# Kernel tuning notes

Hardware: AMD Instinct MI355X
Metric: run time of the kernel (lower is better)

The kernel has to match this reference:

```python
import jax, jax.numpy as jnp
import numpy as np

B, NQ, NK, DQ, DK, DV, H = 8, 256, 512, 256, 256, 256, 64
NEG = -1e6


def setup_inputs() -> dict:
    key = jax.random.key(0)
    k1, k2, k3, k4, k5, k6, k7 = jax.random.split(key, 7)
    return {
        "queries": jax.random.normal(k1, (B, NQ, DQ), dtype=jnp.float32),
        "keys": jax.random.normal(k2, (B, NK, DK), dtype=jnp.float32),
        "values": jax.random.normal(k3, (B, NK, DV), dtype=jnp.float32),
        "valid_lens": jax.random.randint(k4, (B,), 1, NK + 1),
        "Wq": jax.random.normal(k5, (DQ, H), dtype=jnp.float32) / np.sqrt(DQ),
        "Wk": jax.random.normal(k6, (DK, H), dtype=jnp.float32) / np.sqrt(DK),
        "wv": jax.random.normal(k7, (H,), dtype=jnp.float32) / np.sqrt(H),
    }


def reference(queries, keys, values, valid_lens, Wq, Wk, wv):
    # project: [B,NQ,H], [B,NK,H]
    q = jnp.einsum("bqd,dh->bqh", queries, Wq)
    k = jnp.einsum("bkd,dh->bkh", keys, Wk)
    # additive features: [B,NQ,NK,H] -> tanh -> reduce with w_v -> scores [B,NQ,NK]
    features = jnp.tanh(q[:, :, None, :] + k[:, None, :, :])
    scores = jnp.einsum("bqkh,h->bqk", features, wv)
    # masked softmax over key axis (per-batch valid_lens)
    mask = jnp.arange(NK)[None, None, :] < valid_lens[:, None, None]
    scores = jnp.where(mask, scores, NEG)
    attn = jax.nn.softmax(scores, axis=-1)
    # dropout p=0 (eval) -> identity; weighted sum of values [B,NQ,DV]
    return jnp.einsum("bqk,bkv->bqv", attn, values)
```

## Files before the change

kernel.cpp:

```cpp
#include <hip/hip_runtime.h>
#include <hip/hip_bf16.h>

constexpr int B  = 8;
constexpr int NQ = 256;
constexpr int NK = 512;
constexpr int D  = 256;
constexpr int DV = 256;
constexpr int H  = 64;
constexpr float LOG2E = 1.4426950408889634f;
constexpr float CSCALE = 2.f * LOG2E;

constexpr int RPB = 32;

__global__ __launch_bounds__(512) void proj_kernel(
    const float* __restrict__ queries, const float* __restrict__ keys,
    const float* __restrict__ Wq, const float* __restrict__ Wk,
    float* __restrict__ qp, float* __restrict__ kp)
{
    const int r0 = blockIdx.x * RPB;
    const bool isQ = (r0 < B * NQ);
    const float* src = isQ ? queries + (size_t)r0 * D
                           : keys + (size_t)(r0 - B * NQ) * D;
    const float* W   = isQ ? Wq : Wk;
    float* out       = isQ ? qp + (size_t)r0 * H
                           : kp + (size_t)(r0 - B * NQ) * H;

    __shared__ __align__(16) float rows[RPB][D];
#pragma unroll
    for (int j = 0; j < 4; ++j)
        ((float4*)&rows[0][0])[threadIdx.x + j * 512] =
            ((const float4*)src)[threadIdx.x + j * 512];
    __syncthreads();

    const int h = threadIdx.x & 63;
    const int g = threadIdx.x >> 6;
    float s0 = 0.f, s1 = 0.f, s2 = 0.f, s3 = 0.f;
#pragma unroll 2
    for (int d4 = 0; d4 < D / 4; ++d4) {
        float w0 = W[(d4 * 4 + 0) * H + h];
        float w1 = W[(d4 * 4 + 1) * H + h];
        float w2 = W[(d4 * 4 + 2) * H + h];
        float w3 = W[(d4 * 4 + 3) * H + h];
        float4 ra = *(const float4*)&rows[g][d4 * 4];
        float4 rb = *(const float4*)&rows[g + 8][d4 * 4];
        float4 rc = *(const float4*)&rows[g + 16][d4 * 4];
        float4 rd = *(const float4*)&rows[g + 24][d4 * 4];
        s0 = fmaf(ra.x, w0, s0);  s1 = fmaf(rb.x, w0, s1);
        s2 = fmaf(rc.x, w0, s2);  s3 = fmaf(rd.x, w0, s3);
        s0 = fmaf(ra.y, w1, s0);  s1 = fmaf(rb.y, w1, s1);
        s2 = fmaf(rc.y, w1, s2);  s3 = fmaf(rd.y, w1, s3);
        s0 = fmaf(ra.z, w2, s0);  s1 = fmaf(rb.z, w2, s1);
        s2 = fmaf(rc.z, w2, s2);  s3 = fmaf(rd.z, w2, s3);
        s0 = fmaf(ra.w, w3, s0);  s1 = fmaf(rb.w, w3, s1);
        s2 = fmaf(rc.w, w3, s2);  s3 = fmaf(rd.w, w3, s3);
    }
    out[g * H + h]         = s0 * CSCALE;
    out[(g + 8) * H + h]   = s1 * CSCALE;
    out[(g + 16) * H + h]  = s2 * CSCALE;
    out[(g + 24) * H + h]  = s3 * CSCALE;
}

constexpr int KT   = 128;
constexpr int KPAD = 68;
constexpr int QPB  = 8;

#define FMA2(acc, a, v) \
    acc.x = fmaf(a, v.x, acc.x); acc.y = fmaf(a, v.y, acc.y);
#define AVQ(acc, aq) \
    FMA2(acc, aq.x, v0) FMA2(acc, aq.y, v1) FMA2(acc, aq.z, v2) FMA2(acc, aq.w, v3)

__global__ __launch_bounds__(1024, 4) void attn_kernel(
    const float* __restrict__ qp, const float* __restrict__ kp,
    const float* __restrict__ values, const int* __restrict__ valid_lens,
    const float* __restrict__ wv, float* __restrict__ out)
{
    const int b    = blockIdx.x & 7;
    const int q0   = (blockIdx.x >> 3) * QPB;
    const int t    = threadIdx.x;
    const int w    = t >> 6;
    const int l    = t & 63;
    const int qloc = w >> 1;
    const int half = w & 1;

    __shared__ __align__(16) float kT[KT * KPAD];
    __shared__ __align__(16) float qv[QPB][H];
    __shared__ __align__(16) float w2[H];
    __shared__ __align__(16) float rq[QPB];
    __shared__ __align__(16) float sc[QPB][NK];

    if (half == 0)
        qv[qloc][l] = qp[((size_t)b * NQ + q0 + qloc) * H + l];

    const float wvl = wv[l];
    float swv = wvl;
#pragma unroll
    for (int off = 32; off > 0; off >>= 1) swv += __shfl_xor(swv, off);
    if (w == 0) w2[l] = -2.f * wvl;

    const int vlen = valid_lens[b];
    const int ntl  = (vlen + KT - 1) / KT;

    for (int kt = ntl; kt < NK / KT; ++kt)
        sc[qloc][kt * KT + half * 64 + l] = 0.f;

    const float* kb = kp + (size_t)b * NK * H;
    float4 r0 = ((const float4*)kb)[t];
    float4 r1 = ((const float4*)kb)[t + 1024];

    for (int kt = 0; kt < ntl; ++kt) {
        __syncthreads();
        {
            int i4 = t;
            *(float4*)&kT[(i4 >> 4) * KPAD + (i4 & 15) * 4] = r0;
            i4 = t + 1024;
            *(float4*)&kT[(i4 >> 4) * KPAD + (i4 & 15) * 4] = r1;
        }
        if (kt + 1 < ntl) {
            const float* nsrc = kb + (size_t)(kt + 1) * KT * H;
            r0 = ((const float4*)nsrc)[t];
            r1 = ((const float4*)nsrc)[t + 1024];
        }
        __syncthreads();

        const int kg = kt * KT + half * 64 + l;
        if (kt * KT + half * 64 < vlen) {
            const float* qrow = &qv[qloc][0];
            const float* krow = &kT[(half * 64 + l) * KPAD];
            float s0 = 0.f;
#pragma unroll
            for (int h4 = 0; h4 < H / 4; ++h4) {
                float4 qq = *(const float4*)&qrow[h4 * 4];
                float4 ww = *(const float4*)&w2[h4 * 4];
                float4 kk = *(const float4*)&krow[h4 * 4];
                float Ax = __builtin_amdgcn_exp2f(qq.x + kk.x) + 1.f;
                float Ay = __builtin_amdgcn_exp2f(qq.y + kk.y) + 1.f;
                float Az = __builtin_amdgcn_exp2f(qq.z + kk.z) + 1.f;
                float Aw = __builtin_amdgcn_exp2f(qq.w + kk.w) + 1.f;
                float n1 = fmaf(ww.x, Ay, ww.y * Ax);
                float d1 = Ax * Ay;
                float n2 = fmaf(ww.z, Aw, ww.w * Az);
                float d2 = Az * Aw;
                float nq = fmaf(n1, d2, n2 * d1);
                float dq = d1 * d2;
                s0 = fmaf(nq, __builtin_amdgcn_rcpf(dq), s0);
            }
            sc[qloc][kg] = (kg < vlen)
                ? __builtin_amdgcn_exp2f((s0 + swv) * LOG2E) : 0.f;
        } else {
            sc[qloc][kg] = 0.f;
        }
    }
    __syncthreads();

    float sum = 0.f;
#pragma unroll
    for (int j = 0; j < 8; ++j) sum += sc[qloc][l + j * 64];
#pragma unroll
    for (int off = 32; off > 0; off >>= 1) sum += __shfl_xor(sum, off);
    if (half == 0 && l == 0) rq[qloc] = __builtin_amdgcn_rcpf(sum);

    float2 acc0{0,0}, acc1{0,0}, acc2{0,0}, acc3{0,0};
    float2 acc4{0,0}, acc5{0,0}, acc6{0,0}, acc7{0,0};
    const float* Vb = values + (size_t)b * NK * DV + half * 128 + 2 * l;
    const int nchunks = (vlen + 3) >> 2;
    for (int c = qloc; c < nchunks; c += 8) {
        const int k = 4 * c;
        float4 a0 = *(const float4*)&sc[0][k];
        float4 a1 = *(const float4*)&sc[1][k];
        float4 a2 = *(const float4*)&sc[2][k];
        float4 a3 = *(const float4*)&sc[3][k];
        float4 a4 = *(const float4*)&sc[4][k];
        float4 a5 = *(const float4*)&sc[5][k];
        float4 a6 = *(const float4*)&sc[6][k];
        float4 a7 = *(const float4*)&sc[7][k];
        const float* vr = Vb + (size_t)k * DV;
        float2 v0 = *(const float2*)(vr);
        float2 v1 = *(const float2*)(vr + DV);
        float2 v2 = *(const float2*)(vr + 2 * DV);
        float2 v3 = *(const float2*)(vr + 3 * DV);
        AVQ(acc0, a0) AVQ(acc1, a1) AVQ(acc2, a2) AVQ(acc3, a3)
        AVQ(acc4, a4) AVQ(acc5, a5) AVQ(acc6, a6) AVQ(acc7, a7)
    }

    float* pt = kT;
    const int pbase = qloc * 4 * 256 + half * 128 + 2 * l;
    *(float2*)&pt[pbase + 0 * 256] = acc0;
    *(float2*)&pt[pbase + 1 * 256] = acc1;
    *(float2*)&pt[pbase + 2 * 256] = acc2;
    *(float2*)&pt[pbase + 3 * 256] = acc3;
    __syncthreads();
    if (w < 4) {
        float4 r{0,0,0,0};
#pragma unroll
        for (int p = 0; p < 8; ++p) {
            float4 x = *(const float4*)&pt[(p * 4 + w) * 256 + 4 * l];
            r.x += x.x; r.y += x.y; r.z += x.z; r.w += x.w;
        }
        const float s = rq[w];
        r.x *= s; r.y *= s; r.z *= s; r.w *= s;
        *(float4*)&out[((size_t)b * NQ + q0 + w) * DV + 4 * l] = r;
    }
    __syncthreads();
    *(float2*)&pt[pbase + 0 * 256] = acc4;
    *(float2*)&pt[pbase + 1 * 256] = acc5;
    *(float2*)&pt[pbase + 2 * 256] = acc6;
    *(float2*)&pt[pbase + 3 * 256] = acc7;
    __syncthreads();
    if (w < 4) {
        float4 r{0,0,0,0};
#pragma unroll
        for (int p = 0; p < 8; ++p) {
            float4 x = *(const float4*)&pt[(p * 4 + w) * 256 + 4 * l];
            r.x += x.x; r.y += x.y; r.z += x.z; r.w += x.w;
        }
        const float s = rq[4 + w];
        r.x *= s; r.y *= s; r.z *= s; r.w *= s;
        *(float4*)&out[((size_t)b * NQ + q0 + 4 + w) * DV + 4 * l] = r;
    }
}

extern "C" void kernel_launch(void* const* d_in, const int* in_sizes, int n_in,
                              void* d_out, int out_size, void* d_ws, size_t ws_size,
                              hipStream_t stream) {
    const float* queries    = (const float*)d_in[0];
    const float* keys       = (const float*)d_in[1];
    const float* values     = (const float*)d_in[2];
    const int*   valid_lens = (const int*)d_in[3];
    const float* Wq         = (const float*)d_in[4];
    const float* Wk         = (const float*)d_in[5];
    const float* wv         = (const float*)d_in[6];
    float* out = (float*)d_out;

    float* qp = (float*)d_ws;
    float* kp = qp + (size_t)B * NQ * H;

    proj_kernel<<<(B * NQ + B * NK) / RPB, 512, 0, stream>>>(
        queries, keys, Wq, Wk, qp, kp);

    attn_kernel<<<B * (NQ / QPB), 1024, 0, stream>>>(
        qp, kp, values, valid_lens, wv, out);
}
```

Before: 103.2 us.

## Interleave attention-value accumulation with score tiles and simplify tanh reduction

```diff
diff --git a/kernel.cpp b/kernel.cpp
--- a/kernel.cpp
+++ b/kernel.cpp
@@ -35,7 +35,7 @@
     const int h = threadIdx.x & 63;
     const int g = threadIdx.x >> 6;
     float s0 = 0.f, s1 = 0.f, s2 = 0.f, s3 = 0.f;
-#pragma unroll 2
+#pragma unroll 4
     for (int d4 = 0; d4 < D / 4; ++d4) {
         float w0 = W[(d4 * 4 + 0) * H + h];
         float w1 = W[(d4 * 4 + 1) * H + h];
@@ -103,12 +103,39 @@
     for (int kt = ntl; kt < NK / KT; ++kt)
         sc[qloc][kt * KT + half * 64 + l] = 0.f;
 
+    float2 acc0{0,0}, acc1{0,0}, acc2{0,0}, acc3{0,0};
+    float2 acc4{0,0}, acc5{0,0}, acc6{0,0}, acc7{0,0};
+    const float* Vb = values + (size_t)b * NK * DV + half * 128 + 2 * l;
+
+    auto av_tile = [&](int kt) {
+#pragma unroll
+        for (int cc = 0; cc < 4; ++cc) {
+            const int k = kt * KT + 4 * (qloc + 8 * cc);
+            if (k >= vlen) continue;
+            float4 a0 = *(const float4*)&sc[0][k];
+            float4 a1 = *(const float4*)&sc[1][k];
+            float4 a2 = *(const float4*)&sc[2][k];
+            float4 a3 = *(const float4*)&sc[3][k];
+            float4 a4 = *(const float4*)&sc[4][k];
+            float4 a5 = *(const float4*)&sc[5][k];
+            float4 a6 = *(const float4*)&sc[6][k];
+            float4 a7 = *(const float4*)&sc[7][k];
+            const float* vr = Vb + (size_t)k * DV;
+            float2 v0 = *(const float2*)(vr);
+            float2 v1 = *(const float2*)(vr + DV);
+            float2 v2 = *(const float2*)(vr + 2 * DV);
+            float2 v3 = *(const float2*)(vr + 3 * DV);
+            AVQ(acc0, a0) AVQ(acc1, a1) AVQ(acc2, a2) AVQ(acc3, a3)
+            AVQ(acc4, a4) AVQ(acc5, a5) AVQ(acc6, a6) AVQ(acc7, a7)
+        }
+    };
+
     const float* kb = kp + (size_t)b * NK * H;
     float4 r0 = ((const float4*)kb)[t];
     float4 r1 = ((const float4*)kb)[t + 1024];
 
     for (int kt = 0; kt < ntl; ++kt) {
-        __syncthreads();
+        if (kt) __syncthreads();
         {
             int i4 = t;
             *(float4*)&kT[(i4 >> 4) * KPAD + (i4 & 15) * 4] = r0;
@@ -132,55 +159,34 @@
                 float4 qq = *(const float4*)&qrow[h4 * 4];
                 float4 ww = *(const float4*)&w2[h4 * 4];
                 float4 kk = *(const float4*)&krow[h4 * 4];
-                float Ax = __builtin_amdgcn_exp2f(qq.x + kk.x) + 1.f;
-                float Ay = __builtin_amdgcn_exp2f(qq.y + kk.y) + 1.f;
-                float Az = __builtin_amdgcn_exp2f(qq.z + kk.z) + 1.f;
-                float Aw = __builtin_amdgcn_exp2f(qq.w + kk.w) + 1.f;
-                float n1 = fmaf(ww.x, Ay, ww.y * Ax);
-                float d1 = Ax * Ay;
-                float n2 = fmaf(ww.z, Aw, ww.w * Az);
-                float d2 = Az * Aw;
-                float nq = fmaf(n1, d2, n2 * d1);
-                float dq = d1 * d2;
-                s0 = fmaf(nq, __builtin_amdgcn_rcpf(dq), s0);
+                float r;
+                r = __builtin_amdgcn_rcpf(__builtin_amdgcn_exp2f(qq.x + kk.x) + 1.f);
+                s0 = fmaf(ww.x, r, s0);
+                r = __builtin_amdgcn_rcpf(__builtin_amdgcn_exp2f(qq.y + kk.y) + 1.f);
+                s0 = fmaf(ww.y, r, s0);
+                r = __builtin_amdgcn_rcpf(__builtin_amdgcn_exp2f(qq.z + kk.z) + 1.f);
+                s0 = fmaf(ww.z, r, s0);
+                r = __builtin_amdgcn_rcpf(__builtin_amdgcn_exp2f(qq.w + kk.w) + 1.f);
+                s0 = fmaf(ww.w, r, s0);
             }
             sc[qloc][kg] = (kg < vlen)
                 ? __builtin_amdgcn_exp2f((s0 + swv) * LOG2E) : 0.f;
         } else {
             sc[qloc][kg] = 0.f;
         }
-    }
-    __syncthreads();
-
+
+        if (kt > 0) av_tile(kt - 1);
+    }
+    __syncthreads();
+
+    av_tile(ntl - 1);
     float sum = 0.f;
 #pragma unroll
     for (int j = 0; j < 8; ++j) sum += sc[qloc][l + j * 64];
 #pragma unroll
     for (int off = 32; off > 0; off >>= 1) sum += __shfl_xor(sum, off);
     if (half == 0 && l == 0) rq[qloc] = __builtin_amdgcn_rcpf(sum);
-
-    float2 acc0{0,0}, acc1{0,0}, acc2{0,0}, acc3{0,0};
-    float2 acc4{0,0}, acc5{0,0}, acc6{0,0}, acc7{0,0};
-    const float* Vb = values + (size_t)b * NK * DV + half * 128 + 2 * l;
-    const int nchunks = (vlen + 3) >> 2;
-    for (int c = qloc; c < nchunks; c += 8) {
-        const int k = 4 * c;
-        float4 a0 = *(const float4*)&sc[0][k];
-        float4 a1 = *(const float4*)&sc[1][k];
-        float4 a2 = *(const float4*)&sc[2][k];
-        float4 a3 = *(const float4*)&sc[3][k];
-        float4 a4 = *(const float4*)&sc[4][k];
-        float4 a5 = *(const float4*)&sc[5][k];
-        float4 a6 = *(const float4*)&sc[6][k];
-        float4 a7 = *(const float4*)&sc[7][k];
-        const float* vr = Vb + (size_t)k * DV;
-        float2 v0 = *(const float2*)(vr);
-        float2 v1 = *(const float2*)(vr + DV);
-        float2 v2 = *(const float2*)(vr + 2 * DV);
-        float2 v3 = *(const float2*)(vr + 3 * DV);
-        AVQ(acc0, a0) AVQ(acc1, a1) AVQ(acc2, a2) AVQ(acc3, a3)
-        AVQ(acc4, a4) AVQ(acc5, a5) AVQ(acc6, a6) AVQ(acc7, a7)
-    }
+    __syncthreads();
 
     float* pt = kT;
     const int pbase = qloc * 4 * 256 + half * 128 + 2 * l;
```

Result: no change. 103.0 us (-0.2%).
